# Optimization experiments

Measured on AMD Instinct MI355X. Metric: run time of the kernel, lower is better.

The kernel has to match this reference:

```python
import jax, jax.numpy as jnp
import numpy as np

B, T, N_EMBS, HEAD = 8, 2048, 1024, 64


def setup_inputs() -> dict:
    key = jax.random.key(0)
    k1, k2, k3, k4 = jax.random.split(key, 4)
    x = jax.random.normal(k1, (B, T, N_EMBS), dtype=jnp.float32)
    # nn.Linear(n_embs, head_size, bias=False): y = x @ W^T with W [head, n_embs].
    # We store the transposed weight [n_embs, head] directly for clean einsum.
    s = 1.0 / np.sqrt(N_EMBS)
    Wk = jax.random.uniform(k2, (N_EMBS, HEAD), jnp.float32, -s, s)
    Wq = jax.random.uniform(k3, (N_EMBS, HEAD), jnp.float32, -s, s)
    Wv = jax.random.uniform(k4, (N_EMBS, HEAD), jnp.float32, -s, s)
    return {"x": x, "Wk": Wk, "Wq": Wq, "Wv": Wv}


def reference(x, Wk, Wq, Wv):
    # Single causal self-attention head (dropout rate = 0.0).
    k = jnp.einsum("btn,nh->bth", x, Wk)  # [B,T,H]
    q = jnp.einsum("btn,nh->bth", x, Wq)
    v = jnp.einsum("btn,nh->bth", x, Wv)
    scale = k.shape[-1] ** -0.5
    scores = jnp.einsum("bqh,bkh->bqk", q, k) * scale  # [B,T,T]
    t = x.shape[1]
    causal = jnp.tril(jnp.ones((t, t), dtype=bool))
    scores = jnp.where(causal, scores, -jnp.inf)
    attn = jax.nn.softmax(scores, axis=-1)
    return jnp.einsum("bqk,bkh->bqh", attn, v)  # [B,T,H]
```

## Files before the change

### kernel.cpp

```cpp
#include <hip/hip_runtime.h>
#include <math.h>

#define BB 8
#define TT 2048
#define NE 1024
#define HH 64
#define BT (BB * TT)

typedef __attribute__((ext_vector_type(8))) short s8v;
typedef __attribute__((ext_vector_type(4))) float f4v;

__device__ inline unsigned short f2bf(float f) {
  union { float f; unsigned u; } v;
  v.f = f;
  unsigned r = (v.u + 0x7FFFu + ((v.u >> 16) & 1u)) >> 16;
  return (unsigned short)r;
}

__device__ inline unsigned short f2bf_trunc(float f) {
  union { float f; unsigned u; } v;
  v.f = f;
  return (unsigned short)(v.u >> 16);
}

__device__ inline unsigned cvtpk(float lo, float hi) {
  unsigned r;
  asm("v_cvt_pk_bf16_f32 %0, %1, %2" : "=v"(r) : "v"(lo), "v"(hi));
  return r;
}

__device__ inline void glds16(const unsigned short* g, unsigned short* l) {
  __builtin_amdgcn_global_load_lds(
      (const __attribute__((address_space(1))) unsigned*)g,
      (__attribute__((address_space(3))) unsigned*)l, 16, 0, 0);
}

__global__ __launch_bounds__(256) void conv_wt_kernel(
    const float* __restrict__ Wq, const float* __restrict__ Wk,
    const float* __restrict__ Wv, unsigned short* __restrict__ WTswz) {
  const int idx = blockIdx.x * 256 + threadIdx.x;
  const int r = idx >> 7;
  const int c8 = idx & 127;
  const int l8 = (c8 & ~7) | ((c8 & 7) ^ (r & 7));
  const int n0 = l8 * 8;
  const int m = r >> 6, h = r & 63;
  const float* W = (m == 0) ? Wq : (m == 1) ? Wk : Wv;
  unsigned short v[8];
#pragma unroll
  for (int j = 0; j < 8; ++j) v[j] = f2bf(W[(size_t)(n0 + j) * HH + h]);
  *reinterpret_cast<uint4*>(WTswz + (size_t)r * NE + c8 * 8) =
      *reinterpret_cast<const uint4*>(v);
}

__global__ __launch_bounds__(256, 2) void qkv_proj_mfma(
    const float* __restrict__ x, const unsigned short* __restrict__ WTswz,
    unsigned short* __restrict__ Q, unsigned short* __restrict__ K,
    unsigned short* __restrict__ VT) {
  __shared__ __align__(16) unsigned short Abuf[2][32 * 72];
  __shared__ __align__(16) unsigned short Bbuf[2][192 * 64];

  const int tid = threadIdx.x;
  const int lane = tid & 63;
  const int w = tid >> 6;
  const int rg = w & 1, cg = w >> 1;
  const int lr = lane & 15, lg = lane >> 4;
  const int row0 = blockIdx.x * 32;

  const int arow = tid >> 3, aunit = tid & 7;
  const float* __restrict__ xrow = x + (size_t)(row0 + arow) * NE + aunit * 8;
  unsigned short* const awr = &Abuf[0][0] + arow * 72 + aunit * 8;

  const int bcol = w * 48 + (lane >> 3);
  const unsigned short* const bsrc0 =
      WTswz + (size_t)bcol * NE + (lane & 7) * 8;
  unsigned short* const bdst0 = &Bbuf[0][0] + (w * 48) * 64;

  f4v acc[6];
#pragma unroll
  for (int c = 0; c < 6; ++c) acc[c] = (f4v)0.f;

  float4 a0 = *reinterpret_cast<const float4*>(xrow);
  float4 a1 = *reinterpret_cast<const float4*>(xrow + 4);
#pragma unroll
  for (int j = 0; j < 6; ++j)
    glds16(bsrc0 + (size_t)j * 8 * NE, bdst0 + j * 512);
  {
    unsigned au[4] = {cvtpk(a0.x, a0.y), cvtpk(a0.z, a0.w),
                      cvtpk(a1.x, a1.y), cvtpk(a1.z, a1.w)};
    *reinterpret_cast<uint4*>(awr) = *reinterpret_cast<const uint4*>(au);
  }
  __syncthreads();

  int cur = 0;
  for (int t = 0; t < 16; ++t) {
    const int kcn = (t + 1) * 64;
    if (t < 15) {
      a0 = *reinterpret_cast<const float4*>(xrow + kcn);
      a1 = *reinterpret_cast<const float4*>(xrow + kcn + 4);
#pragma unroll
      for (int j = 0; j < 6; ++j)
        glds16(bsrc0 + (size_t)j * 8 * NE + kcn,
               bdst0 + (cur ^ 1) * 12288 + j * 512);
    }
    const unsigned short* Ab = &Abuf[cur][0];
    const unsigned short* Bb = &Bbuf[cur][0];
#pragma unroll
    for (int ks = 0; ks < 2; ++ks) {
      const s8v a = *reinterpret_cast<const s8v*>(
          Ab + (rg * 16 + lr) * 72 + ks * 32 + lg * 8);
#pragma unroll
      for (int c = 0; c < 6; ++c) {
        const int col = cg * 96 + c * 16 + lr;
        const int uraw = (lg + ks * 4) ^ (lr & 7);
        const s8v b = *reinterpret_cast<const s8v*>(Bb + col * 64 + uraw * 8);
        acc[c] = __builtin_amdgcn_mfma_f32_16x16x32_bf16(a, b, acc[c], 0, 0, 0);
      }
    }
    if (t < 15) {
      unsigned au[4] = {cvtpk(a0.x, a0.y), cvtpk(a0.z, a0.w),
                        cvtpk(a1.x, a1.y), cvtpk(a1.z, a1.w)};
      *reinterpret_cast<uint4*>(awr + (cur ^ 1) * 2304) =
          *reinterpret_cast<const uint4*>(au);
      __syncthreads();
      cur ^= 1;
    }
  }

  const float QSCL = 0.18033688011112042f;
#pragma unroll
  for (int c = 0; c < 6; ++c) {
    const int col = cg * 96 + c * 16 + lr;
    const int m = col >> 6;
    const int h = col & 63;
#pragma unroll
    for (int r = 0; r < 4; ++r) {
      const int rr = row0 + rg * 16 + lg * 4 + r;
      if (m == 0) {
        Q[(size_t)rr * HH + h] = f2bf(acc[c][r] * QSCL);
      } else if (m == 1) {
        K[(size_t)rr * HH + h] = f2bf(acc[c][r]);
      } else {
        const int bb = rr >> 11, tt2 = rr & (TT - 1);
        VT[((size_t)bb * HH + h) * TT + tt2] = f2bf(acc[c][r]);
      }
    }
  }
}

__global__ __launch_bounds__(256, 4) void flash_attn_mfma(
    const unsigned short* __restrict__ Q, const unsigned short* __restrict__ K,
    const unsigned short* __restrict__ VT, float* __restrict__ out) {
  __shared__ unsigned short pl[4][16][72];
  __shared__ float ol[4][16][64];
  __shared__ float ml[4][16];
  __shared__ float ll[4][16];

  const int tid = threadIdx.x;
  const int lane = tid & 63;
  const int w = tid >> 6;
  const int lr = lane & 15;
  const int lg = lane >> 4;
  const int bid = blockIdx.x;
  const int b = bid & 7;
  const int qt = 127 - (bid >> 3);
  const int q0 = qt * 16;
  const size_t rowbase = (size_t)b * TT;

  const int nt = (qt >> 2) + 1;
  const int base = nt >> 2, rem = nt & 3;
  const int t0 = w * base + (w < rem ? w : rem);
  const int cnt = base + (w < rem ? 1 : 0);

  const s8v qf0 = *reinterpret_cast<const s8v*>(
      Q + (rowbase + q0 + lr) * HH + lg * 8);
  const s8v qf1 = *reinterpret_cast<const s8v*>(
      Q + (rowbase + q0 + lr) * HH + 32 + lg * 8);

  f4v o[4];
#pragma unroll
  for (int n = 0; n < 4; ++n) o[n] = (f4v)0.f;
  float mrow[4], lrow[4];
#pragma unroll
  for (int r = 0; r < 4; ++r) { mrow[r] = -INFINITY; lrow[r] = 0.f; }

  for (int kt = t0; kt < t0 + cnt; ++kt) {
    const int k0 = kt * 64;
    f4v s[4];
#pragma unroll
    for (int nk = 0; nk < 4; ++nk) s[nk] = (f4v)0.f;
    __builtin_amdgcn_s_setprio(1);
#pragma unroll
    for (int nk = 0; nk < 4; ++nk) {
      const unsigned short* kp = K + (rowbase + k0 + 16 * nk + lr) * HH + lg * 8;
      const s8v kf0 = *reinterpret_cast<const s8v*>(kp);
      const s8v kf1 = *reinterpret_cast<const s8v*>(kp + 32);
      s[nk] = __builtin_amdgcn_mfma_f32_16x16x32_bf16(qf0, kf0, s[nk], 0, 0, 0);
      s[nk] = __builtin_amdgcn_mfma_f32_16x16x32_bf16(qf1, kf1, s[nk], 0, 0, 0);
    }
    __builtin_amdgcn_s_setprio(0);
    s8v vfr[2][4];
#pragma unroll
    for (int kh = 0; kh < 2; ++kh)
#pragma unroll
      for (int n = 0; n < 4; ++n)
        vfr[kh][n] = *reinterpret_cast<const s8v*>(
            VT + ((size_t)b * HH + 16 * n + lr) * TT + k0 + kh * 32 + lg * 8);

    if (kt == nt - 1) {
#pragma unroll
      for (int nk = 0; nk < 4; ++nk) {
        const int kk = k0 + 16 * nk + lr;
#pragma unroll
        for (int r = 0; r < 4; ++r) {
          const int qq = q0 + lg * 4 + r;
          if (kk > qq) s[nk][r] = -INFINITY;
        }
      }
    }

    float mx_[4];
    float grow = -INFINITY;
#pragma unroll
    for (int r = 0; r < 4; ++r) {
      float mx = fmaxf(fmaxf(s[0][r], s[1][r]), fmaxf(s[2][r], s[3][r]));
#pragma unroll
      for (int off = 1; off < 16; off <<= 1)
        mx = fmaxf(mx, __shfl_xor(mx, off));
      mx_[r] = mx;
      grow = fmaxf(grow, mx - mrow[r]);
    }
    if (!__all(grow <= 8.f)) {
#pragma unroll
      for (int r = 0; r < 4; ++r) {
        const float mnew = fmaxf(mrow[r], mx_[r]);
        const float scl = exp2f(mrow[r] - mnew);
        mrow[r] = mnew;
        lrow[r] *= scl;
#pragma unroll
        for (int n = 0; n < 4; ++n) o[n][r] *= scl;
      }
    }
#pragma unroll
    for (int r = 0; r < 4; ++r) {
      float rs = 0.f;
#pragma unroll
      for (int nk = 0; nk < 4; ++nk) {
        const float p = exp2f(s[nk][r] - mrow[r]);
        s[nk][r] = p;
        rs += p;
      }
#pragma unroll
      for (int off = 1; off < 16; off <<= 1)
        rs += __shfl_xor(rs, off);
      lrow[r] += rs;
    }
#pragma unroll
    for (int nk = 0; nk < 4; ++nk)
#pragma unroll
      for (int r = 0; r < 4; ++r)
        pl[w][lg * 4 + r][16 * nk + lr] = f2bf_trunc(s[nk][r]);
#pragma unroll
    for (int kh = 0; kh < 2; ++kh) {
      const int pc = kh * 32 + lg * 8;
      const ushort4 plo = *reinterpret_cast<const ushort4*>(&pl[w][lr][pc]);
      const ushort4 phi = *reinterpret_cast<const ushort4*>(&pl[w][lr][pc + 4]);
      s8v pa;
      pa[0] = plo.x; pa[1] = plo.y; pa[2] = plo.z; pa[3] = plo.w;
      pa[4] = phi.x; pa[5] = phi.y; pa[6] = phi.z; pa[7] = phi.w;
      __builtin_amdgcn_s_setprio(1);
#pragma unroll
      for (int n = 0; n < 4; ++n)
        o[n] = __builtin_amdgcn_mfma_f32_16x16x32_bf16(pa, vfr[kh][n], o[n], 0, 0, 0);
      __builtin_amdgcn_s_setprio(0);
    }
  }

#pragma unroll
  for (int n = 0; n < 4; ++n)
#pragma unroll
    for (int r = 0; r < 4; ++r) ol[w][lg * 4 + r][16 * n + lr] = o[n][r];
  if (lr == 0) {
#pragma unroll
    for (int r = 0; r < 4; ++r) {
      ml[w][lg * 4 + r] = mrow[r];
      ll[w][lg * 4 + r] = lrow[r];
    }
  }
  __syncthreads();

  const int row = tid >> 4;
  const int c0 = (tid & 15) * 4;
  float m0 = ml[0][row], m1 = ml[1][row], m2 = ml[2][row], m3 = ml[3][row];
  const float ms = fmaxf(fmaxf(m0, m1), fmaxf(m2, m3));
  const float w0 = exp2f(m0 - ms), w1 = exp2f(m1 - ms);
  const float w2 = exp2f(m2 - ms), w3 = exp2f(m3 - ms);
  const float lsum = w0 * ll[0][row] + w1 * ll[1][row] +
                     w2 * ll[2][row] + w3 * ll[3][row];
  float4 osum;
  osum.x = w0 * ol[0][row][c0 + 0] + w1 * ol[1][row][c0 + 0] +
           w2 * ol[2][row][c0 + 0] + w3 * ol[3][row][c0 + 0];
  osum.y = w0 * ol[0][row][c0 + 1] + w1 * ol[1][row][c0 + 1] +
           w2 * ol[2][row][c0 + 1] + w3 * ol[3][row][c0 + 1];
  osum.z = w0 * ol[0][row][c0 + 2] + w1 * ol[1][row][c0 + 2] +
           w2 * ol[2][row][c0 + 2] + w3 * ol[3][row][c0 + 2];
  osum.w = w0 * ol[0][row][c0 + 3] + w1 * ol[1][row][c0 + 3] +
           w2 * ol[2][row][c0 + 3] + w3 * ol[3][row][c0 + 3];
  const float inv = 1.0f / lsum;
  float4 res;
  res.x = osum.x * inv; res.y = osum.y * inv;
  res.z = osum.z * inv; res.w = osum.w * inv;
  *reinterpret_cast<float4*>(out + (rowbase + q0 + row) * HH + c0) = res;
}

extern "C" void kernel_launch(void* const* d_in, const int* in_sizes, int n_in,
                              void* d_out, int out_size, void* d_ws, size_t ws_size,
                              hipStream_t stream) {
  const float* x  = (const float*)d_in[0];
  const float* Wk = (const float*)d_in[1];
  const float* Wq = (const float*)d_in[2];
  const float* Wv = (const float*)d_in[3];
  float* out = (float*)d_out;

  unsigned short* ws = (unsigned short*)d_ws;
  unsigned short* Q  = ws;
  unsigned short* K  = ws + (size_t)BT * HH;
  unsigned short* VT = ws + 2 * (size_t)BT * HH;
  unsigned short* WT = ws + 3 * (size_t)BT * HH;

  conv_wt_kernel<<<96, 256, 0, stream>>>(Wq, Wk, Wv, WT);
  qkv_proj_mfma<<<512, 256, 0, stream>>>(x, WT, Q, K, VT);
  flash_attn_mfma<<<1024, 256, 0, stream>>>(Q, K, VT, out);
}
```

Before: 73.00 us.

## Drop LDS staging in QKV projection and prefetch K tiles in attention

The QKV projection no longer stages through shared memory. Weights are pre-laid out in MFMA fragment order, and x and W fragments are loaded straight into registers with a multi-slot software prefetch; occupancy is raised to 4 blocks. The attention kernel double-buffers K fragments across iterations and computes the softmax row sum with an extra MFMA against a ones vector instead of shuffle reductions. Its occupancy bound is lowered to 3. The trade-offs are higher register pressure and a row sum now taken from bf16-truncated probabilities.

```diff
diff --git a/kernel.cpp b/kernel.cpp
--- a/kernel.cpp
+++ b/kernel.cpp
@@ -29,101 +29,74 @@
   return r;
 }
 
-__device__ inline void glds16(const unsigned short* g, unsigned short* l) {
-  __builtin_amdgcn_global_load_lds(
-      (const __attribute__((address_space(1))) unsigned*)g,
-      (__attribute__((address_space(3))) unsigned*)l, 16, 0, 0);
-}
-
 __global__ __launch_bounds__(256) void conv_wt_kernel(
     const float* __restrict__ Wq, const float* __restrict__ Wk,
-    const float* __restrict__ Wv, unsigned short* __restrict__ WTswz) {
+    const float* __restrict__ Wv, unsigned short* __restrict__ WTf) {
   const int idx = blockIdx.x * 256 + threadIdx.x;
-  const int r = idx >> 7;
-  const int c8 = idx & 127;
-  const int l8 = (c8 & ~7) | ((c8 & 7) ^ (r & 7));
-  const int n0 = l8 * 8;
-  const int m = r >> 6, h = r & 63;
+  const int cb = idx >> 11;
+  const int ks = (idx >> 6) & 31;
+  const int lane = idx & 63;
+  const int lr = lane & 15, lg = lane >> 4;
+  const int col = cb * 16 + lr;
+  const int m = col >> 6, h = col & 63;
+  const int n0 = ks * 32 + lg * 8;
   const float* W = (m == 0) ? Wq : (m == 1) ? Wk : Wv;
   unsigned short v[8];
 #pragma unroll
   for (int j = 0; j < 8; ++j) v[j] = f2bf(W[(size_t)(n0 + j) * HH + h]);
-  *reinterpret_cast<uint4*>(WTswz + (size_t)r * NE + c8 * 8) =
+  *reinterpret_cast<uint4*>(WTf + (size_t)idx * 8) =
       *reinterpret_cast<const uint4*>(v);
 }
 
-__global__ __launch_bounds__(256, 2) void qkv_proj_mfma(
-    const float* __restrict__ x, const unsigned short* __restrict__ WTswz,
+__global__ __launch_bounds__(256, 4) void qkv_proj_mfma(
+    const float* __restrict__ x, const unsigned short* __restrict__ WTf,
     unsigned short* __restrict__ Q, unsigned short* __restrict__ K,
     unsigned short* __restrict__ VT) {
-  __shared__ __align__(16) unsigned short Abuf[2][32 * 72];
-  __shared__ __align__(16) unsigned short Bbuf[2][192 * 64];
-
   const int tid = threadIdx.x;
   const int lane = tid & 63;
   const int w = tid >> 6;
   const int rg = w & 1, cg = w >> 1;
   const int lr = lane & 15, lg = lane >> 4;
-  const int row0 = blockIdx.x * 32;
-
-  const int arow = tid >> 3, aunit = tid & 7;
-  const float* __restrict__ xrow = x + (size_t)(row0 + arow) * NE + aunit * 8;
-  unsigned short* const awr = &Abuf[0][0] + arow * 72 + aunit * 8;
-
-  const int bcol = w * 48 + (lane >> 3);
-  const unsigned short* const bsrc0 =
-      WTswz + (size_t)bcol * NE + (lane & 7) * 8;
-  unsigned short* const bdst0 = &Bbuf[0][0] + (w * 48) * 64;
+  const int row0 = blockIdx.x * 32 + rg * 16;
+
+  const unsigned xoff = (unsigned)(row0 + lr) * NE + lg * 8;
+  unsigned boff[6];
+#pragma unroll
+  for (int c = 0; c < 6; ++c)
+    boff[c] = (unsigned)(cg * 6 + c) * 16384 + lane * 8;
 
   f4v acc[6];
 #pragma unroll
   for (int c = 0; c < 6; ++c) acc[c] = (f4v)0.f;
 
-  float4 a0 = *reinterpret_cast<const float4*>(xrow);
-  float4 a1 = *reinterpret_cast<const float4*>(xrow + 4);
-#pragma unroll
-  for (int j = 0; j < 6; ++j)
-    glds16(bsrc0 + (size_t)j * 8 * NE, bdst0 + j * 512);
-  {
-    unsigned au[4] = {cvtpk(a0.x, a0.y), cvtpk(a0.z, a0.w),
-                      cvtpk(a1.x, a1.y), cvtpk(a1.z, a1.w)};
-    *reinterpret_cast<uint4*>(awr) = *reinterpret_cast<const uint4*>(au);
-  }
-  __syncthreads();
-
-  int cur = 0;
-  for (int t = 0; t < 16; ++t) {
-    const int kcn = (t + 1) * 64;
-    if (t < 15) {
-      a0 = *reinterpret_cast<const float4*>(xrow + kcn);
-      a1 = *reinterpret_cast<const float4*>(xrow + kcn + 4);
-#pragma unroll
-      for (int j = 0; j < 6; ++j)
-        glds16(bsrc0 + (size_t)j * 8 * NE + kcn,
-               bdst0 + (cur ^ 1) * 12288 + j * 512);
-    }
-    const unsigned short* Ab = &Abuf[cur][0];
-    const unsigned short* Bb = &Bbuf[cur][0];
-#pragma unroll
-    for (int ks = 0; ks < 2; ++ks) {
-      const s8v a = *reinterpret_cast<const s8v*>(
-          Ab + (rg * 16 + lr) * 72 + ks * 32 + lg * 8);
-#pragma unroll
-      for (int c = 0; c < 6; ++c) {
-        const int col = cg * 96 + c * 16 + lr;
-        const int uraw = (lg + ks * 4) ^ (lr & 7);
-        const s8v b = *reinterpret_cast<const s8v*>(Bb + col * 64 + uraw * 8);
-        acc[c] = __builtin_amdgcn_mfma_f32_16x16x32_bf16(a, b, acc[c], 0, 0, 0);
-      }
-    }
-    if (t < 15) {
-      unsigned au[4] = {cvtpk(a0.x, a0.y), cvtpk(a0.z, a0.w),
-                        cvtpk(a1.x, a1.y), cvtpk(a1.z, a1.w)};
-      *reinterpret_cast<uint4*>(awr + (cur ^ 1) * 2304) =
-          *reinterpret_cast<const uint4*>(au);
-      __syncthreads();
-      cur ^= 1;
-    }
+  float4 ab[4][2];
+  s8v bb[2][6];
+
+  auto LOADA = [&](int sl, int ks) {
+    ab[sl][0] = *reinterpret_cast<const float4*>(x + xoff + ks * 32);
+    ab[sl][1] = *reinterpret_cast<const float4*>(x + xoff + ks * 32 + 4);
+  };
+  auto LOADB = [&](int sl, int ks) {
+#pragma unroll
+    for (int c = 0; c < 6; ++c)
+      bb[sl][c] = *reinterpret_cast<const s8v*>(WTf + boff[c] + ks * 512);
+  };
+
+  LOADA(0, 0); LOADA(1, 1); LOADA(2, 2);
+  LOADB(0, 0);
+#pragma unroll
+  for (int ks = 0; ks < 32; ++ks) {
+    if (ks + 3 < 32) LOADA((ks + 3) & 3, ks + 3);
+    if (ks + 1 < 32) LOADB((ks + 1) & 1, ks + 1);
+    const int sa = ks & 3, sb = ks & 1;
+    union { unsigned u[4]; s8v v; } au;
+    au.u[0] = cvtpk(ab[sa][0].x, ab[sa][0].y);
+    au.u[1] = cvtpk(ab[sa][0].z, ab[sa][0].w);
+    au.u[2] = cvtpk(ab[sa][1].x, ab[sa][1].y);
+    au.u[3] = cvtpk(ab[sa][1].z, ab[sa][1].w);
+#pragma unroll
+    for (int c = 0; c < 6; ++c)
+      acc[c] = __builtin_amdgcn_mfma_f32_16x16x32_bf16(au.v, bb[sb][c], acc[c], 0, 0, 0);
   }
 
   const float QSCL = 0.18033688011112042f;
@@ -134,20 +107,20 @@
     const int h = col & 63;
 #pragma unroll
     for (int r = 0; r < 4; ++r) {
-      const int rr = row0 + rg * 16 + lg * 4 + r;
+      const int rr = row0 + lg * 4 + r;
       if (m == 0) {
         Q[(size_t)rr * HH + h] = f2bf(acc[c][r] * QSCL);
       } else if (m == 1) {
         K[(size_t)rr * HH + h] = f2bf(acc[c][r]);
       } else {
-        const int bb = rr >> 11, tt2 = rr & (TT - 1);
-        VT[((size_t)bb * HH + h) * TT + tt2] = f2bf(acc[c][r]);
+        const int bb2 = rr >> 11, tt2 = rr & (TT - 1);
+        VT[((size_t)bb2 * HH + h) * TT + tt2] = f2bf(acc[c][r]);
       }
     }
   }
 }
 
-__global__ __launch_bounds__(256, 4) void flash_attn_mfma(
+__global__ __launch_bounds__(256, 3) void flash_attn_mfma(
     const unsigned short* __restrict__ Q, const unsigned short* __restrict__ K,
     const unsigned short* __restrict__ VT, float* __restrict__ out) {
   __shared__ unsigned short pl[4][16][72];
@@ -169,21 +142,38 @@
   const int nt = (qt >> 2) + 1;
   const int base = nt >> 2, rem = nt & 3;
   const int t0 = w * base + (w < rem ? w : rem);
-  const int cnt = base + (w < rem ? 1 : 0);
+  const int kend = t0 + base + (w < rem ? 1 : 0);
 
   const s8v qf0 = *reinterpret_cast<const s8v*>(
       Q + (rowbase + q0 + lr) * HH + lg * 8);
   const s8v qf1 = *reinterpret_cast<const s8v*>(
       Q + (rowbase + q0 + lr) * HH + 32 + lg * 8);
 
-  f4v o[4];
-#pragma unroll
-  for (int n = 0; n < 4; ++n) o[n] = (f4v)0.f;
-  float mrow[4], lrow[4];
-#pragma unroll
-  for (int r = 0; r < 4; ++r) { mrow[r] = -INFINITY; lrow[r] = 0.f; }
-
-  for (int kt = t0; kt < t0 + cnt; ++kt) {
+  s8v vone;
+#pragma unroll
+  for (int j = 0; j < 8; ++j) vone[j] = (short)0x3F80;
+
+  f4v o[5];
+#pragma unroll
+  for (int n = 0; n < 5; ++n) o[n] = (f4v)0.f;
+  float mrow[4];
+#pragma unroll
+  for (int r = 0; r < 4; ++r) mrow[r] = -INFINITY;
+
+  const unsigned short* const Kb = K + rowbase * HH;
+
+  s8v kfX[2][4], kfY[2][4];
+  auto LOADK = [&](s8v (&kf)[2][4], int kt) {
+    const int k0 = kt * 64;
+#pragma unroll
+    for (int nk = 0; nk < 4; ++nk) {
+      const unsigned short* kp = Kb + (size_t)(k0 + 16 * nk + lr) * HH + lg * 8;
+      kf[0][nk] = *reinterpret_cast<const s8v*>(kp);
+      kf[1][nk] = *reinterpret_cast<const s8v*>(kp + 32);
+    }
+  };
+
+  auto PROCESS = [&](const s8v (&kf)[2][4], int kt) {
     const int k0 = kt * 64;
     f4v s[4];
 #pragma unroll
@@ -191,11 +181,8 @@
     __builtin_amdgcn_s_setprio(1);
 #pragma unroll
     for (int nk = 0; nk < 4; ++nk) {
-      const unsigned short* kp = K + (rowbase + k0 + 16 * nk + lr) * HH + lg * 8;
-      const s8v kf0 = *reinterpret_cast<const s8v*>(kp);
-      const s8v kf1 = *reinterpret_cast<const s8v*>(kp + 32);
-      s[nk] = __builtin_amdgcn_mfma_f32_16x16x32_bf16(qf0, kf0, s[nk], 0, 0, 0);
-      s[nk] = __builtin_amdgcn_mfma_f32_16x16x32_bf16(qf1, kf1, s[nk], 0, 0, 0);
+      s[nk] = __builtin_amdgcn_mfma_f32_16x16x32_bf16(qf0, kf[0][nk], s[nk], 0, 0, 0);
+      s[nk] = __builtin_amdgcn_mfma_f32_16x16x32_bf16(qf1, kf[1][nk], s[nk], 0, 0, 0);
     }
     __builtin_amdgcn_s_setprio(0);
     s8v vfr[2][4];
@@ -235,30 +222,15 @@
         const float mnew = fmaxf(mrow[r], mx_[r]);
         const float scl = exp2f(mrow[r] - mnew);
         mrow[r] = mnew;
-        lrow[r] *= scl;
-#pragma unroll
-        for (int n = 0; n < 4; ++n) o[n][r] *= scl;
+#pragma unroll
+        for (int n = 0; n < 5; ++n) o[n][r] *= scl;
       }
     }
 #pragma unroll
-    for (int r = 0; r < 4; ++r) {
-      float rs = 0.f;
-#pragma unroll
-      for (int nk = 0; nk < 4; ++nk) {
-        const float p = exp2f(s[nk][r] - mrow[r]);
-        s[nk][r] = p;
-        rs += p;
-      }
-#pragma unroll
-      for (int off = 1; off < 16; off <<= 1)
-        rs += __shfl_xor(rs, off);
-      lrow[r] += rs;
-    }
-#pragma unroll
     for (int nk = 0; nk < 4; ++nk)
 #pragma unroll
       for (int r = 0; r < 4; ++r)
-        pl[w][lg * 4 + r][16 * nk + lr] = f2bf_trunc(s[nk][r]);
+        pl[w][lg * 4 + r][16 * nk + lr] = f2bf_trunc(exp2f(s[nk][r] - mrow[r]));
 #pragma unroll
     for (int kh = 0; kh < 2; ++kh) {
       const int pc = kh * 32 + lg * 8;
@@ -271,9 +243,21 @@
 #pragma unroll
       for (int n = 0; n < 4; ++n)
         o[n] = __builtin_amdgcn_mfma_f32_16x16x32_bf16(pa, vfr[kh][n], o[n], 0, 0, 0);
+      o[4] = __builtin_amdgcn_mfma_f32_16x16x32_bf16(pa, vone, o[4], 0, 0, 0);
       __builtin_amdgcn_s_setprio(0);
     }
+  };
+
+  int kt = t0;
+  if (kt < kend) LOADK(kfX, kt);
+  while (kt + 2 <= kend) {
+    LOADK(kfY, kt + 1);
+    PROCESS(kfX, kt);
+    if (kt + 2 < kend) LOADK(kfX, kt + 2);
+    PROCESS(kfY, kt + 1);
+    kt += 2;
   }
+  if (kt < kend) PROCESS(kfX, kt);
 
 #pragma unroll
   for (int n = 0; n < 4; ++n)
@@ -283,7 +267,7 @@
 #pragma unroll
     for (int r = 0; r < 4; ++r) {
       ml[w][lg * 4 + r] = mrow[r];
-      ll[w][lg * 4 + r] = lrow[r];
+      ll[w][lg * 4 + r] = o[4][r];
     }
   }
   __syncthreads();
```

New measurement: 91.62 us. 1.26x slower.
